# Kernel tuning notes

Measured on AMD Instinct MI355X. Metric: run time of the kernel, lower is better.

Reference implementation:

```python
import jax, jax.numpy as jnp
import numpy as np
import math

IN_CH = 256
RED_CH = 32  # max(256//8, 32)

def setup_inputs() -> dict:
    key = jax.random.key(0)
    k1, k2, k3, k4, k5 = jax.random.split(key, 5)
    x = jax.random.normal(k1, (2, IN_CH, 8, 28, 28), dtype=jnp.float32)
    # 1x1x1 Conv3d weights, kaiming-normal style scale (fan_out)
    def kaiming(k, shape):
        fan_out = shape[0]
        std = math.sqrt(2.0 / fan_out)
        return jax.random.normal(k, shape, dtype=jnp.float32) * std
    q_w = kaiming(k2, (RED_CH, IN_CH))
    k_w = kaiming(k3, (RED_CH, IN_CH))
    v_w = kaiming(k4, (RED_CH, IN_CH))
    out_w = kaiming(k5, (IN_CH, RED_CH))
    return {"x": x, "q_w": q_w, "k_w": k_w, "v_w": v_w, "out_w": out_w}

def reference(x, q_w, k_w, v_w, out_w):
    b, c, t, h, w = x.shape
    n = t * h * w
    xf = x.reshape(b, c, n)  # [B, C, N] (1x1x1 conv == channel matmul)
    q = jnp.einsum('rc,bcn->brn', q_w, xf)  # [B, Cr, N]
    k = jnp.einsum('rc,bcn->brn', k_w, xf)
    v = jnp.einsum('rc,bcn->brn', v_w, xf)
    scale = 1.0 / math.sqrt(RED_CH)
    attn = jnp.einsum('bri,brj->bij', q, k) * scale  # [B, N, N]
    attn = jax.nn.softmax(attn, axis=2)
    out = jnp.einsum('brj,bij->bri', v, attn)  # [B, Cr, N]
    out = jnp.einsum('cr,brn->bcn', out_w, out).reshape(b, c, t, h, w)
    return x + out
```

## Files before the change

### kernel.cpp

```cpp
#include <hip/hip_runtime.h>
#include <hip/hip_bf16.h>

#define NPOS 6272
#define NT   98
#define CIN  256
#define CR   32
#define BATCH 2
#define QS2  0.25503371989518595f
#define PPITCH 72

typedef short bf16x8s __attribute__((ext_vector_type(8)));
typedef short short4v __attribute__((ext_vector_type(4)));
typedef float f32x4   __attribute__((ext_vector_type(4)));
typedef unsigned short ushort_t;

__device__ __forceinline__ ushort_t f2bf(float f) {
    unsigned u = __builtin_bit_cast(unsigned, f);
    u += 0x7fff + ((u >> 16) & 1);
    return (ushort_t)(u >> 16);
}
__device__ __forceinline__ float bf2f(ushort_t h) {
    return __builtin_bit_cast(float, (unsigned)h << 16);
}

__global__ __launch_bounds__(256) void qkv_kernel(
    const float* __restrict__ x, const float* __restrict__ qw,
    const float* __restrict__ kw, const float* __restrict__ vw,
    ushort_t* __restrict__ Qh, ushort_t* __restrict__ Ql,
    ushort_t* __restrict__ Kh, ushort_t* __restrict__ Kl,
    ushort_t* __restrict__ Vt)
{
    const int b   = blockIdx.y;
    const int z   = blockIdx.z;
    const int nl  = threadIdx.x & 63;
    const int n   = blockIdx.x * 64 + nl;
    const int g   = __builtin_amdgcn_readfirstlane(threadIdx.x >> 6);
    const float* w  = (z == 0) ? qw : (z == 1) ? kw : vw;
    const float* xb = x + (size_t)b * CIN * NPOS + n;

    float acc[8];
#pragma unroll
    for (int i = 0; i < 8; ++i) acc[i] = 0.f;
#pragma unroll 8
    for (int c = 0; c < CIN; ++c) {
        float xv = xb[(size_t)c * NPOS];
#pragma unroll
        for (int i = 0; i < 8; ++i)
            acc[i] += w[(g * 8 + i) * CIN + c] * xv;
    }
    if (z == 2) {
#pragma unroll
        for (int i = 0; i < 8; ++i)
            Vt[((size_t)b * CR + g * 8 + i) * NPOS + n] = f2bf(acc[i]);
    } else {
        ushort_t* dh = (z == 0) ? Qh : Kh;
        ushort_t* dl = (z == 0) ? Ql : Kl;
        float s = (z == 0) ? QS2 : 1.0f;
        bf16x8s fh, fl;
#pragma unroll
        for (int i = 0; i < 8; ++i) {
            float v = acc[i] * s;
            ushort_t h = f2bf(v);
            fh[i] = (short)h;
            fl[i] = (short)f2bf(v - bf2f(h));
        }
        size_t off = ((size_t)b * NPOS + n) * CR + g * 8;
        *(bf16x8s*)(dh + off) = fh;
        *(bf16x8s*)(dl + off) = fl;
    }
}

__global__ __launch_bounds__(64, 4) void attn_kernel(
    const ushort_t* __restrict__ Qh, const ushort_t* __restrict__ Ql,
    const ushort_t* __restrict__ Kh, const ushort_t* __restrict__ Kl,
    const ushort_t* __restrict__ Vt, ushort_t* __restrict__ Opart,
    float* __restrict__ Mp, float* __restrict__ Lp, int iters)
{
    __shared__ __align__(16) ushort_t pbuf[2 * 16 * PPITCH];

    const int lane = threadIdx.x;
    const int col  = lane & 15;
    const int quad = lane >> 4;
    const int b    = blockIdx.z;
    const int s    = blockIdx.y;
    const int qw0  = blockIdx.x * 32;

    const ushort_t* Qhb = Qh + (size_t)b * NPOS * CR;
    const ushort_t* Qlb = Ql + (size_t)b * NPOS * CR;
    const ushort_t* Khb = Kh + (size_t)b * NPOS * CR;
    const ushort_t* Klb = Kl + (size_t)b * NPOS * CR;
    const ushort_t* Vtb = Vt + (size_t)b * CR * NPOS;

    bf16x8s qbh[2], qbl[2];
    qbh[0] = *(const bf16x8s*)(Qhb + (size_t)(qw0 + col) * CR + quad * 8);
    qbh[1] = *(const bf16x8s*)(Qhb + (size_t)(qw0 + 16 + col) * CR + quad * 8);
    qbl[0] = *(const bf16x8s*)(Qlb + (size_t)(qw0 + col) * CR + quad * 8);
    qbl[1] = *(const bf16x8s*)(Qlb + (size_t)(qw0 + 16 + col) * CR + quad * 8);

    f32x4 oc[2][2];
#pragma unroll
    for (int h = 0; h < 2; ++h)
#pragma unroll
        for (int c = 0; c < 2; ++c)
#pragma unroll
            for (int r = 0; r < 4; ++r) oc[h][c][r] = 0.f;
    float m_[2] = { -1e30f, -1e30f };
    float l_[2] = { 0.f, 0.f };

    for (int it = 0; it < iters; ++it) {
        const int j0 = (s * iters + it) * 64;
        bf16x8s kh[4], kl[4], vb[2][2];
#pragma unroll
        for (int f = 0; f < 4; ++f) {
            kh[f] = *(const bf16x8s*)(Khb + (size_t)(j0 + f * 16 + col) * CR + quad * 8);
            kl[f] = *(const bf16x8s*)(Klb + (size_t)(j0 + f * 16 + col) * CR + quad * 8);
        }
#pragma unroll
        for (int k2 = 0; k2 < 2; ++k2)
#pragma unroll
            for (int c = 0; c < 2; ++c)
                vb[k2][c] = *(const bf16x8s*)(Vtb + (size_t)(c * 16 + col) * NPOS
                                              + j0 + k2 * 32 + quad * 8);

        f32x4 z4; z4[0] = 0.f; z4[1] = 0.f; z4[2] = 0.f; z4[3] = 0.f;
#pragma unroll
        for (int h = 0; h < 2; ++h) {
            f32x4 sc[4];
#pragma unroll
            for (int f = 0; f < 4; ++f) {
                sc[f] = __builtin_amdgcn_mfma_f32_16x16x32_bf16(kl[f], qbh[h], z4, 0, 0, 0);
                sc[f] = __builtin_amdgcn_mfma_f32_16x16x32_bf16(kh[f], qbl[h], sc[f], 0, 0, 0);
                sc[f] = __builtin_amdgcn_mfma_f32_16x16x32_bf16(kh[f], qbh[h], sc[f], 0, 0, 0);
            }
            float v0 = fmaxf(fmaxf(sc[0][0], sc[0][1]), fmaxf(sc[0][2], sc[0][3]));
            float v1 = fmaxf(fmaxf(sc[1][0], sc[1][1]), fmaxf(sc[1][2], sc[1][3]));
            float v2 = fmaxf(fmaxf(sc[2][0], sc[2][1]), fmaxf(sc[2][2], sc[2][3]));
            float v3 = fmaxf(fmaxf(sc[3][0], sc[3][1]), fmaxf(sc[3][2], sc[3][3]));
            float v  = fmaxf(fmaxf(v0, v1), fmaxf(v2, v3));
            v = fmaxf(v, __shfl_xor(v, 16));
            v = fmaxf(v, __shfl_xor(v, 32));
            float mo = m_[h];
            float mn = fmaxf(mo, v);
            float al = __builtin_amdgcn_exp2f(mo - mn);
            float lsum = 0.f;
#pragma unroll
            for (int f = 0; f < 4; ++f) {
                float p0 = __builtin_amdgcn_exp2f(sc[f][0] - mn);
                float p1 = __builtin_amdgcn_exp2f(sc[f][1] - mn);
                float p2 = __builtin_amdgcn_exp2f(sc[f][2] - mn);
                float p3 = __builtin_amdgcn_exp2f(sc[f][3] - mn);
                lsum += (p0 + p1) + (p2 + p3);
                short4v pk;
                pk[0] = (short)f2bf(p0); pk[1] = (short)f2bf(p1);
                pk[2] = (short)f2bf(p2); pk[3] = (short)f2bf(p3);
                *(short4v*)(&pbuf[h * 16 * PPITCH + col * PPITCH + f * 16 + quad * 4]) = pk;
            }
            m_[h] = mn;
            l_[h] = l_[h] * al + lsum;
#pragma unroll
            for (int r = 0; r < 4; ++r) { oc[h][0][r] *= al; oc[h][1][r] *= al; }
        }
#pragma unroll
        for (int h = 0; h < 2; ++h) {
#pragma unroll
            for (int k2 = 0; k2 < 2; ++k2) {
                bf16x8s pb = *(const bf16x8s*)(
                    &pbuf[h * 16 * PPITCH + col * PPITCH + k2 * 32 + quad * 8]);
                oc[h][0] = __builtin_amdgcn_mfma_f32_16x16x32_bf16(vb[k2][0], pb, oc[h][0], 0, 0, 0);
                oc[h][1] = __builtin_amdgcn_mfma_f32_16x16x32_bf16(vb[k2][1], pb, oc[h][1], 0, 0, 0);
            }
        }
    }

#pragma unroll
    for (int h = 0; h < 2; ++h) {
        float l = l_[h];
        l += __shfl_xor(l, 16);
        l += __shfl_xor(l, 32);
        l_[h] = l;
    }

    const size_t sb = (size_t)(s * BATCH + b);
    ushort_t* Ob = Opart + sb * CR * NPOS;
#pragma unroll
    for (int h = 0; h < 2; ++h)
#pragma unroll
        for (int c = 0; c < 2; ++c)
#pragma unroll
            for (int r = 0; r < 4; ++r) {
                int ch = c * 16 + quad * 4 + r;
                Ob[(size_t)ch * NPOS + qw0 + h * 16 + col] = f2bf(oc[h][c][r]);
            }
    if (quad == 0) {
#pragma unroll
        for (int h = 0; h < 2; ++h) {
            Mp[sb * NPOS + qw0 + h * 16 + col] = m_[h];
            Lp[sb * NPOS + qw0 + h * 16 + col] = l_[h];
        }
    }
}

template <int S_>
__global__ __launch_bounds__(256) void merge_kernel(
    const ushort_t* __restrict__ Opart, const float* __restrict__ Mp,
    const float* __restrict__ Lp, float* __restrict__ Omrg)
{
    const int b  = blockIdx.y;
    const int z  = blockIdx.z;
    const int nl = threadIdx.x & 63;
    const int n  = blockIdx.x * 64 + nl;
    const int g  = __builtin_amdgcn_readfirstlane(threadIdx.x >> 6);
    const int r  = z * 4 + g;

    float mg = -1e30f;
#pragma unroll
    for (int s = 0; s < S_; ++s)
        mg = fmaxf(mg, Mp[(size_t)(s * BATCH + b) * NPOS + n]);
    float lg = 0.f, acc = 0.f;
#pragma unroll
    for (int s = 0; s < S_; ++s) {
        size_t sb = (size_t)(s * BATCH + b);
        float w = __builtin_amdgcn_exp2f(Mp[sb * NPOS + n] - mg);
        lg  += w * Lp[sb * NPOS + n];
        acc += w * bf2f(Opart[(sb * CR + r) * NPOS + n]);
    }
    Omrg[((size_t)b * CR + r) * NPOS + n] = acc / lg;
}

__global__ __launch_bounds__(256) void proj_kernel(
    const float* __restrict__ Omrg, const float* __restrict__ ow,
    const float* __restrict__ x, float* __restrict__ y)
{
    const int b  = blockIdx.y;
    const int z  = blockIdx.z;
    const int nl = threadIdx.x & 63;
    const int n  = blockIdx.x * 64 + nl;
    const int g  = __builtin_amdgcn_readfirstlane(threadIdx.x >> 6);

    float o[CR];
#pragma unroll
    for (int r = 0; r < CR; ++r)
        o[r] = Omrg[((size_t)b * CR + r) * NPOS + n];

    const float* xb = x + (size_t)b * CIN * NPOS + n;
    float*       yb = y + (size_t)b * CIN * NPOS + n;
    const int c0 = z * 32 + g * 8;
#pragma unroll
    for (int cc = 0; cc < 8; ++cc) {
        int c = c0 + cc;
        float acc = xb[(size_t)c * NPOS];
#pragma unroll
        for (int r = 0; r < CR; ++r) acc += ow[c * CR + r] * o[r];
        yb[(size_t)c * NPOS] = acc;
    }
}

extern "C" void kernel_launch(void* const* d_in, const int* in_sizes, int n_in,
                              void* d_out, int out_size, void* d_ws, size_t ws_size,
                              hipStream_t stream)
{
    const float* x  = (const float*)d_in[0];
    const float* qw = (const float*)d_in[1];
    const float* kw = (const float*)d_in[2];
    const float* vw = (const float*)d_in[3];
    const float* ow = (const float*)d_in[4];
    float* out = (float*)d_out;

    const size_t qkvN = (size_t)BATCH * CR * NPOS;
    const int s_cand[4] = {14, 7, 2, 1};
    int S = 1;
    for (int i = 0; i < 4; ++i) {
        int Sc = s_cand[i];
        size_t need = 5 * qkvN * sizeof(ushort_t)
                    + qkvN * sizeof(float)
                    + (size_t)Sc * qkvN * sizeof(ushort_t)
                    + 2 * (size_t)Sc * BATCH * NPOS * sizeof(float);
        if (need <= ws_size) { S = Sc; break; }
    }
    ushort_t* Qh = (ushort_t*)d_ws;
    ushort_t* Ql = Qh + qkvN;
    ushort_t* Kh = Ql + qkvN;
    ushort_t* Kl = Kh + qkvN;
    ushort_t* Vt = Kl + qkvN;
    float* Omrg  = (float*)(Vt + qkvN);
    ushort_t* Op = (ushort_t*)(Omrg + qkvN);
    float* Mp    = (float*)(Op + (size_t)S * qkvN);
    float* Lp    = Mp + (size_t)S * BATCH * NPOS;
    const int iters = NPOS / (S * 64);

    qkv_kernel<<<dim3(NT, BATCH, 3), 256, 0, stream>>>(x, qw, kw, vw,
                                                       Qh, Ql, Kh, Kl, Vt);
    attn_kernel<<<dim3(196, S, BATCH), 64, 0, stream>>>(Qh, Ql, Kh, Kl, Vt,
                                                        Op, Mp, Lp, iters);
    dim3 mg(NT, BATCH, 8);
    switch (S) {
        case 14: merge_kernel<14><<<mg, 256, 0, stream>>>(Op, Mp, Lp, Omrg); break;
        case 7:  merge_kernel<7> <<<mg, 256, 0, stream>>>(Op, Mp, Lp, Omrg); break;
        case 2:  merge_kernel<2> <<<mg, 256, 0, stream>>>(Op, Mp, Lp, Omrg); break;
        default: merge_kernel<1> <<<mg, 256, 0, stream>>>(Op, Mp, Lp, Omrg); break;
    }
    proj_kernel<<<dim3(NT, BATCH, 8), 256, 0, stream>>>(Omrg, ow, x, out);
}
```

Before: 152.9 us.

## Use two-wave attention blocks, compile-time iteration count, and batched QKV loads

```diff
diff --git a/kernel.cpp b/kernel.cpp
--- a/kernel.cpp
+++ b/kernel.cpp
@@ -23,7 +23,7 @@
     return __builtin_bit_cast(float, (unsigned)h << 16);
 }
 
-__global__ __launch_bounds__(256) void qkv_kernel(
+__global__ __launch_bounds__(256, 4) void qkv_kernel(
     const float* __restrict__ x, const float* __restrict__ qw,
     const float* __restrict__ kw, const float* __restrict__ vw,
     ushort_t* __restrict__ Qh, ushort_t* __restrict__ Ql,
@@ -36,17 +36,23 @@
     const int n   = blockIdx.x * 64 + nl;
     const int g   = __builtin_amdgcn_readfirstlane(threadIdx.x >> 6);
     const float* w  = (z == 0) ? qw : (z == 1) ? kw : vw;
+    const float* wr = w + g * 8 * CIN;
     const float* xb = x + (size_t)b * CIN * NPOS + n;
 
     float acc[8];
 #pragma unroll
     for (int i = 0; i < 8; ++i) acc[i] = 0.f;
-#pragma unroll 8
-    for (int c = 0; c < CIN; ++c) {
-        float xv = xb[(size_t)c * NPOS];
-#pragma unroll
-        for (int i = 0; i < 8; ++i)
-            acc[i] += w[(g * 8 + i) * CIN + c] * xv;
+#pragma unroll 2
+    for (int cb = 0; cb < CIN; cb += 16) {
+        float xv[16];
+#pragma unroll
+        for (int i = 0; i < 16; ++i)
+            xv[i] = xb[(size_t)(cb + i) * NPOS];
+#pragma unroll
+        for (int i = 0; i < 16; ++i)
+#pragma unroll
+            for (int r = 0; r < 8; ++r)
+                acc[r] += wr[r * CIN + cb + i] * xv[i];
     }
     if (z == 2) {
 #pragma unroll
@@ -70,20 +76,23 @@
     }
 }
 
-__global__ __launch_bounds__(64, 4) void attn_kernel(
+template <int ITERS>
+__global__ __launch_bounds__(128, 3) void attn_kernel(
     const ushort_t* __restrict__ Qh, const ushort_t* __restrict__ Ql,
     const ushort_t* __restrict__ Kh, const ushort_t* __restrict__ Kl,
     const ushort_t* __restrict__ Vt, ushort_t* __restrict__ Opart,
-    float* __restrict__ Mp, float* __restrict__ Lp, int iters)
-{
-    __shared__ __align__(16) ushort_t pbuf[2 * 16 * PPITCH];
-
-    const int lane = threadIdx.x;
+    float* __restrict__ Mp, float* __restrict__ Lp)
+{
+    __shared__ __align__(16) ushort_t pbuf[2 * 2 * 16 * PPITCH];
+
+    const int lane = threadIdx.x & 63;
+    const int wv   = threadIdx.x >> 6;
     const int col  = lane & 15;
     const int quad = lane >> 4;
     const int b    = blockIdx.z;
     const int s    = blockIdx.y;
-    const int qw0  = blockIdx.x * 32;
+    const int qw0  = blockIdx.x * 64 + wv * 32;
+    ushort_t* pb   = &pbuf[wv * 2 * 16 * PPITCH];
 
     const ushort_t* Qhb = Qh + (size_t)b * NPOS * CR;
     const ushort_t* Qlb = Ql + (size_t)b * NPOS * CR;
@@ -107,8 +116,9 @@
     float m_[2] = { -1e30f, -1e30f };
     float l_[2] = { 0.f, 0.f };
 
-    for (int it = 0; it < iters; ++it) {
-        const int j0 = (s * iters + it) * 64;
+#pragma unroll 7
+    for (int it = 0; it < ITERS; ++it) {
+        const int j0 = (s * ITERS + it) * 64;
         bf16x8s kh[4], kl[4], vb[2][2];
 #pragma unroll
         for (int f = 0; f < 4; ++f) {
@@ -153,7 +163,7 @@
                 short4v pk;
                 pk[0] = (short)f2bf(p0); pk[1] = (short)f2bf(p1);
                 pk[2] = (short)f2bf(p2); pk[3] = (short)f2bf(p3);
-                *(short4v*)(&pbuf[h * 16 * PPITCH + col * PPITCH + f * 16 + quad * 4]) = pk;
+                *(short4v*)(&pb[h * 16 * PPITCH + col * PPITCH + f * 16 + quad * 4]) = pk;
             }
             m_[h] = mn;
             l_[h] = l_[h] * al + lsum;
@@ -164,10 +174,10 @@
         for (int h = 0; h < 2; ++h) {
 #pragma unroll
             for (int k2 = 0; k2 < 2; ++k2) {
-                bf16x8s pb = *(const bf16x8s*)(
-                    &pbuf[h * 16 * PPITCH + col * PPITCH + k2 * 32 + quad * 8]);
-                oc[h][0] = __builtin_amdgcn_mfma_f32_16x16x32_bf16(vb[k2][0], pb, oc[h][0], 0, 0, 0);
-                oc[h][1] = __builtin_amdgcn_mfma_f32_16x16x32_bf16(vb[k2][1], pb, oc[h][1], 0, 0, 0);
+                bf16x8s pbo = *(const bf16x8s*)(
+                    &pb[h * 16 * PPITCH + col * PPITCH + k2 * 32 + quad * 8]);
+                oc[h][0] = __builtin_amdgcn_mfma_f32_16x16x32_bf16(vb[k2][0], pbo, oc[h][0], 0, 0, 0);
+                oc[h][1] = __builtin_amdgcn_mfma_f32_16x16x32_bf16(vb[k2][1], pbo, oc[h][1], 0, 0, 0);
             }
         }
     }
@@ -286,12 +296,16 @@
     ushort_t* Op = (ushort_t*)(Omrg + qkvN);
     float* Mp    = (float*)(Op + (size_t)S * qkvN);
     float* Lp    = Mp + (size_t)S * BATCH * NPOS;
-    const int iters = NPOS / (S * 64);
 
     qkv_kernel<<<dim3(NT, BATCH, 3), 256, 0, stream>>>(x, qw, kw, vw,
                                                        Qh, Ql, Kh, Kl, Vt);
-    attn_kernel<<<dim3(196, S, BATCH), 64, 0, stream>>>(Qh, Ql, Kh, Kl, Vt,
-                                                        Op, Mp, Lp, iters);
+    dim3 ag(NT, S, BATCH);
+    switch (S) {
+        case 14: attn_kernel<7> <<<ag, 128, 0, stream>>>(Qh, Ql, Kh, Kl, Vt, Op, Mp, Lp); break;
+        case 7:  attn_kernel<14><<<ag, 128, 0, stream>>>(Qh, Ql, Kh, Kl, Vt, Op, Mp, Lp); break;
+        case 2:  attn_kernel<49><<<ag, 128, 0, stream>>>(Qh, Ql, Kh, Kl, Vt, Op, Mp, Lp); break;
+        default: attn_kernel<98><<<ag, 128, 0, stream>>>(Qh, Ql, Kh, Kl, Vt, Op, Mp, Lp); break;
+    }
     dim3 mg(NT, BATCH, 8);
     switch (S) {
         case 14: merge_kernel<14><<<mg, 256, 0, stream>>>(Op, Mp, Lp, Omrg); break;
```

Result: slower. 163.3 us (+6.8%).

## Prefetch KV tiles in attention, skip rescale, fuse merge with projection

Applied to the files above, without the earlier changes.

```diff
diff --git a/kernel.cpp b/kernel.cpp
--- a/kernel.cpp
+++ b/kernel.cpp
@@ -70,11 +70,94 @@
     }
 }
 
-__global__ __launch_bounds__(64, 4) void attn_kernel(
+struct KVTile {
+    bf16x8s kh[4], kl[4], vb[4];
+};
+
+__device__ __forceinline__ KVTile load_tile(
+    const ushort_t* __restrict__ Khb, const ushort_t* __restrict__ Klb,
+    const ushort_t* __restrict__ Vtb, int j0, int col, int quad)
+{
+    KVTile t;
+#pragma unroll
+    for (int f = 0; f < 4; ++f) {
+        t.kh[f] = *(const bf16x8s*)(Khb + (size_t)(j0 + f * 16 + col) * CR + quad * 8);
+        t.kl[f] = *(const bf16x8s*)(Klb + (size_t)(j0 + f * 16 + col) * CR + quad * 8);
+    }
+#pragma unroll
+    for (int k2 = 0; k2 < 2; ++k2)
+#pragma unroll
+        for (int c = 0; c < 2; ++c)
+            t.vb[k2 * 2 + c] = *(const bf16x8s*)(
+                Vtb + (size_t)(c * 16 + col) * NPOS + j0 + k2 * 32 + quad * 8);
+    return t;
+}
+
+__device__ __forceinline__ void compute_tile(
+    const KVTile& t, const bf16x8s* qbh, const bf16x8s* qbl,
+    f32x4 (&oc)[2][2], float (&m_)[2], float (&l_)[2],
+    ushort_t* pb, int col, int quad)
+{
+    f32x4 z4 = {0.f, 0.f, 0.f, 0.f};
+#pragma unroll
+    for (int h = 0; h < 2; ++h) {
+        f32x4 sc[4];
+#pragma unroll
+        for (int f = 0; f < 4; ++f) {
+            sc[f] = __builtin_amdgcn_mfma_f32_16x16x32_bf16(t.kl[f], qbh[h], z4, 0, 0, 0);
+            sc[f] = __builtin_amdgcn_mfma_f32_16x16x32_bf16(t.kh[f], qbl[h], sc[f], 0, 0, 0);
+            sc[f] = __builtin_amdgcn_mfma_f32_16x16x32_bf16(t.kh[f], qbh[h], sc[f], 0, 0, 0);
+        }
+        float v0 = fmaxf(fmaxf(sc[0][0], sc[0][1]), fmaxf(sc[0][2], sc[0][3]));
+        float v1 = fmaxf(fmaxf(sc[1][0], sc[1][1]), fmaxf(sc[1][2], sc[1][3]));
+        float v2 = fmaxf(fmaxf(sc[2][0], sc[2][1]), fmaxf(sc[2][2], sc[2][3]));
+        float v3 = fmaxf(fmaxf(sc[3][0], sc[3][1]), fmaxf(sc[3][2], sc[3][3]));
+        float v  = fmaxf(fmaxf(v0, v1), fmaxf(v2, v3));
+        v = fmaxf(v, __shfl_xor(v, 16));
+        v = fmaxf(v, __shfl_xor(v, 32));
+        float mo = m_[h];
+        if (__any(v > mo)) {
+            float mn = fmaxf(mo, v);
+            float al = __builtin_amdgcn_exp2f(mo - mn);
+            l_[h] *= al;
+#pragma unroll
+            for (int r = 0; r < 4; ++r) { oc[h][0][r] *= al; oc[h][1][r] *= al; }
+            m_[h] = mn;
+        }
+        float mn = m_[h];
+        float lsum = 0.f;
+#pragma unroll
+        for (int f = 0; f < 4; ++f) {
+            float p0 = __builtin_amdgcn_exp2f(sc[f][0] - mn);
+            float p1 = __builtin_amdgcn_exp2f(sc[f][1] - mn);
+            float p2 = __builtin_amdgcn_exp2f(sc[f][2] - mn);
+            float p3 = __builtin_amdgcn_exp2f(sc[f][3] - mn);
+            lsum += (p0 + p1) + (p2 + p3);
+            short4v pk;
+            pk[0] = (short)f2bf(p0); pk[1] = (short)f2bf(p1);
+            pk[2] = (short)f2bf(p2); pk[3] = (short)f2bf(p3);
+            *(short4v*)(&pb[h * 16 * PPITCH + col * PPITCH + f * 16 + quad * 4]) = pk;
+        }
+        l_[h] += lsum;
+    }
+#pragma unroll
+    for (int h = 0; h < 2; ++h) {
+#pragma unroll
+        for (int k2 = 0; k2 < 2; ++k2) {
+            bf16x8s pbo = *(const bf16x8s*)(
+                &pb[h * 16 * PPITCH + col * PPITCH + k2 * 32 + quad * 8]);
+            oc[h][0] = __builtin_amdgcn_mfma_f32_16x16x32_bf16(t.vb[k2 * 2 + 0], pbo, oc[h][0], 0, 0, 0);
+            oc[h][1] = __builtin_amdgcn_mfma_f32_16x16x32_bf16(t.vb[k2 * 2 + 1], pbo, oc[h][1], 0, 0, 0);
+        }
+    }
+}
+
+template <int ITERS>
+__global__ __launch_bounds__(64, 3) void attn_kernel(
     const ushort_t* __restrict__ Qh, const ushort_t* __restrict__ Ql,
     const ushort_t* __restrict__ Kh, const ushort_t* __restrict__ Kl,
     const ushort_t* __restrict__ Vt, ushort_t* __restrict__ Opart,
-    float* __restrict__ Mp, float* __restrict__ Lp, int iters)
+    float* __restrict__ Mp, float* __restrict__ Lp)
 {
     __shared__ __align__(16) ushort_t pbuf[2 * 16 * PPITCH];
 
@@ -84,6 +167,7 @@
     const int b    = blockIdx.z;
     const int s    = blockIdx.y;
     const int qw0  = blockIdx.x * 32;
+    ushort_t* pb   = pbuf;
 
     const ushort_t* Qhb = Qh + (size_t)b * NPOS * CR;
     const ushort_t* Qlb = Ql + (size_t)b * NPOS * CR;
@@ -107,68 +191,20 @@
     float m_[2] = { -1e30f, -1e30f };
     float l_[2] = { 0.f, 0.f };
 
-    for (int it = 0; it < iters; ++it) {
-        const int j0 = (s * iters + it) * 64;
-        bf16x8s kh[4], kl[4], vb[2][2];
-#pragma unroll
-        for (int f = 0; f < 4; ++f) {
-            kh[f] = *(const bf16x8s*)(Khb + (size_t)(j0 + f * 16 + col) * CR + quad * 8);
-            kl[f] = *(const bf16x8s*)(Klb + (size_t)(j0 + f * 16 + col) * CR + quad * 8);
-        }
-#pragma unroll
-        for (int k2 = 0; k2 < 2; ++k2)
-#pragma unroll
-            for (int c = 0; c < 2; ++c)
-                vb[k2][c] = *(const bf16x8s*)(Vtb + (size_t)(c * 16 + col) * NPOS
-                                              + j0 + k2 * 32 + quad * 8);
-
-        f32x4 z4; z4[0] = 0.f; z4[1] = 0.f; z4[2] = 0.f; z4[3] = 0.f;
-#pragma unroll
-        for (int h = 0; h < 2; ++h) {
-            f32x4 sc[4];
-#pragma unroll
-            for (int f = 0; f < 4; ++f) {
-                sc[f] = __builtin_amdgcn_mfma_f32_16x16x32_bf16(kl[f], qbh[h], z4, 0, 0, 0);
-                sc[f] = __builtin_amdgcn_mfma_f32_16x16x32_bf16(kh[f], qbl[h], sc[f], 0, 0, 0);
-                sc[f] = __builtin_amdgcn_mfma_f32_16x16x32_bf16(kh[f], qbh[h], sc[f], 0, 0, 0);
-            }
-            float v0 = fmaxf(fmaxf(sc[0][0], sc[0][1]), fmaxf(sc[0][2], sc[0][3]));
-            float v1 = fmaxf(fmaxf(sc[1][0], sc[1][1]), fmaxf(sc[1][2], sc[1][3]));
-            float v2 = fmaxf(fmaxf(sc[2][0], sc[2][1]), fmaxf(sc[2][2], sc[2][3]));
-            float v3 = fmaxf(fmaxf(sc[3][0], sc[3][1]), fmaxf(sc[3][2], sc[3][3]));
-            float v  = fmaxf(fmaxf(v0, v1), fmaxf(v2, v3));
-            v = fmaxf(v, __shfl_xor(v, 16));
-            v = fmaxf(v, __shfl_xor(v, 32));
-            float mo = m_[h];
-            float mn = fmaxf(mo, v);
-            float al = __builtin_amdgcn_exp2f(mo - mn);
-            float lsum = 0.f;
-#pragma unroll
-            for (int f = 0; f < 4; ++f) {
-                float p0 = __builtin_amdgcn_exp2f(sc[f][0] - mn);
-                float p1 = __builtin_amdgcn_exp2f(sc[f][1] - mn);
-                float p2 = __builtin_amdgcn_exp2f(sc[f][2] - mn);
-                float p3 = __builtin_amdgcn_exp2f(sc[f][3] - mn);
-                lsum += (p0 + p1) + (p2 + p3);
-                short4v pk;
-                pk[0] = (short)f2bf(p0); pk[1] = (short)f2bf(p1);
-                pk[2] = (short)f2bf(p2); pk[3] = (short)f2bf(p3);
-                *(short4v*)(&pbuf[h * 16 * PPITCH + col * PPITCH + f * 16 + quad * 4]) = pk;
-            }
-            m_[h] = mn;
-            l_[h] = l_[h] * al + lsum;
-#pragma unroll
-            for (int r = 0; r < 4; ++r) { oc[h][0][r] *= al; oc[h][1][r] *= al; }
-        }
-#pragma unroll
-        for (int h = 0; h < 2; ++h) {
-#pragma unroll
-            for (int k2 = 0; k2 < 2; ++k2) {
-                bf16x8s pb = *(const bf16x8s*)(
-                    &pbuf[h * 16 * PPITCH + col * PPITCH + k2 * 32 + quad * 8]);
-                oc[h][0] = __builtin_amdgcn_mfma_f32_16x16x32_bf16(vb[k2][0], pb, oc[h][0], 0, 0, 0);
-                oc[h][1] = __builtin_amdgcn_mfma_f32_16x16x32_bf16(vb[k2][1], pb, oc[h][1], 0, 0, 0);
-            }
+    if constexpr (ITERS <= 14) {
+        KVTile cur = load_tile(Khb, Klb, Vtb, s * ITERS * 64, col, quad);
+#pragma unroll
+        for (int it = 0; it < ITERS; ++it) {
+            KVTile nxt = cur;
+            if (it + 1 < ITERS)
+                nxt = load_tile(Khb, Klb, Vtb, (s * ITERS + it + 1) * 64, col, quad);
+            compute_tile(cur, qbh, qbl, oc, m_, l_, pb, col, quad);
+            cur = nxt;
+        }
+    } else {
+        for (int it = 0; it < ITERS; ++it) {
+            KVTile cur = load_tile(Khb, Klb, Vtb, (s * ITERS + it) * 64, col, quad);
+            compute_tile(cur, qbh, qbl, oc, m_, l_, pb, col, quad);
         }
     }
 
@@ -201,52 +237,51 @@
 }
 
 template <int S_>
-__global__ __launch_bounds__(256) void merge_kernel(
+__global__ __launch_bounds__(64, 4) void mergeproj_kernel(
     const ushort_t* __restrict__ Opart, const float* __restrict__ Mp,
-    const float* __restrict__ Lp, float* __restrict__ Omrg)
+    const float* __restrict__ Lp, const float* __restrict__ ow,
+    const float* __restrict__ x, float* __restrict__ y)
 {
     const int b  = blockIdx.y;
     const int z  = blockIdx.z;
-    const int nl = threadIdx.x & 63;
-    const int n  = blockIdx.x * 64 + nl;
-    const int g  = __builtin_amdgcn_readfirstlane(threadIdx.x >> 6);
-    const int r  = z * 4 + g;
+    const int n  = blockIdx.x * 64 + threadIdx.x;
 
     float mg = -1e30f;
 #pragma unroll
     for (int s = 0; s < S_; ++s)
         mg = fmaxf(mg, Mp[(size_t)(s * BATCH + b) * NPOS + n]);
-    float lg = 0.f, acc = 0.f;
+    float wseg[S_];
+    float lg = 0.f;
 #pragma unroll
     for (int s = 0; s < S_; ++s) {
         size_t sb = (size_t)(s * BATCH + b);
         float w = __builtin_amdgcn_exp2f(Mp[sb * NPOS + n] - mg);
-        lg  += w * Lp[sb * NPOS + n];
-        acc += w * bf2f(Opart[(sb * CR + r) * NPOS + n]);
-    }
-    Omrg[((size_t)b * CR + r) * NPOS + n] = acc / lg;
-}
-
-__global__ __launch_bounds__(256) void proj_kernel(
-    const float* __restrict__ Omrg, const float* __restrict__ ow,
-    const float* __restrict__ x, float* __restrict__ y)
-{
-    const int b  = blockIdx.y;
-    const int z  = blockIdx.z;
-    const int nl = threadIdx.x & 63;
-    const int n  = blockIdx.x * 64 + nl;
-    const int g  = __builtin_amdgcn_readfirstlane(threadIdx.x >> 6);
+        wseg[s] = w;
+        lg += w * Lp[sb * NPOS + n];
+    }
+    float inv = 1.f / lg;
 
     float o[CR];
 #pragma unroll
-    for (int r = 0; r < CR; ++r)
-        o[r] = Omrg[((size_t)b * CR + r) * NPOS + n];
+    for (int r = 0; r < CR; ++r) o[r] = 0.f;
+#pragma unroll
+    for (int s = 0; s < S_; ++s) {
+        const ushort_t* Ob = Opart + (size_t)(s * BATCH + b) * CR * NPOS + n;
+        float ov[CR];
+#pragma unroll
+        for (int r = 0; r < CR; ++r)
+            ov[r] = bf2f(Ob[(size_t)r * NPOS]);
+#pragma unroll
+        for (int r = 0; r < CR; ++r) o[r] += wseg[s] * ov[r];
+    }
+#pragma unroll
+    for (int r = 0; r < CR; ++r) o[r] *= inv;
 
     const float* xb = x + (size_t)b * CIN * NPOS + n;
     float*       yb = y + (size_t)b * CIN * NPOS + n;
-    const int c0 = z * 32 + g * 8;
-#pragma unroll
-    for (int cc = 0; cc < 8; ++cc) {
+    const int c0 = z * 64;
+#pragma unroll 8
+    for (int cc = 0; cc < 64; ++cc) {
         int c = c0 + cc;
         float acc = xb[(size_t)c * NPOS];
 #pragma unroll
@@ -272,7 +307,6 @@
     for (int i = 0; i < 4; ++i) {
         int Sc = s_cand[i];
         size_t need = 5 * qkvN * sizeof(ushort_t)
-                    + qkvN * sizeof(float)
                     + (size_t)Sc * qkvN * sizeof(ushort_t)
                     + 2 * (size_t)Sc * BATCH * NPOS * sizeof(float);
         if (need <= ws_size) { S = Sc; break; }
@@ -282,22 +316,24 @@
     ushort_t* Kh = Ql + qkvN;
     ushort_t* Kl = Kh + qkvN;
     ushort_t* Vt = Kl + qkvN;
-    float* Omrg  = (float*)(Vt + qkvN);
-    ushort_t* Op = (ushort_t*)(Omrg + qkvN);
+    ushort_t* Op = Vt + qkvN;
     float* Mp    = (float*)(Op + (size_t)S * qkvN);
     float* Lp    = Mp + (size_t)S * BATCH * NPOS;
-    const int iters = NPOS / (S * 64);
 
     qkv_kernel<<<dim3(NT, BATCH, 3), 256, 0, stream>>>(x, qw, kw, vw,
                                                        Qh, Ql, Kh, Kl, Vt);
-    attn_kernel<<<dim3(196, S, BATCH), 64, 0, stream>>>(Qh, Ql, Kh, Kl, Vt,
-                                                        Op, Mp, Lp, iters);
-    dim3 mg(NT, BATCH, 8);
+    dim3 ag(196, S, BATCH);
     switch (S) {
-        case 14: merge_kernel<14><<<mg, 256, 0, stream>>>(Op, Mp, Lp, Omrg); break;
-        case 7:  merge_kernel<7> <<<mg, 256, 0, stream>>>(Op, Mp, Lp, Omrg); break;
-        case 2:  merge_kernel<2> <<<mg, 256, 0, stream>>>(Op, Mp, Lp, Omrg); break;
-        default: merge_kernel<1> <<<mg, 256, 0, stream>>>(Op, Mp, Lp, Omrg); break;
-    }
-    proj_kernel<<<dim3(NT, BATCH, 8), 256, 0, stream>>>(Omrg, ow, x, out);
-}
+        case 14: attn_kernel<7> <<<ag, 64, 0, stream>>>(Qh, Ql, Kh, Kl, Vt, Op, Mp, Lp); break;
+        case 7:  attn_kernel<14><<<ag, 64, 0, stream>>>(Qh, Ql, Kh, Kl, Vt, Op, Mp, Lp); break;
+        case 2:  attn_kernel<49><<<ag, 64, 0, stream>>>(Qh, Ql, Kh, Kl, Vt, Op, Mp, Lp); break;
+        default: attn_kernel<98><<<ag, 64, 0, stream>>>(Qh, Ql, Kh, Kl, Vt, Op, Mp, Lp); break;
+    }
+    dim3 mp(NT, BATCH, 4);
+    switch (S) {
+        case 14: mergeproj_kernel<14><<<mp, 64, 0, stream>>>(Op, Mp, Lp, ow, x, out); break;
+        case 7:  mergeproj_kernel<7> <<<mp, 64, 0, stream>>>(Op, Mp, Lp, ow, x, out); break;
+        case 2:  mergeproj_kernel<2> <<<mp, 64, 0, stream>>>(Op, Mp, Lp, ow, x, out); break;
+        default: mergeproj_kernel<1> <<<mp, 64, 0, stream>>>(Op, Mp, Lp, ow, x, out); break;
+    }
+}
```

Measured after the change: 216.9 us. 1.42x slower.
